# Kernel tuning notes

Hardware: AMD Instinct MI355X
Metric: run time of the kernel (lower is better)

Reference implementation:

```python
import jax, jax.numpy as jnp
import numpy as np


def setup_inputs() -> dict:
    key = jax.random.key(0)
    k1, k2 = jax.random.split(key)
    B, Te, Td, D = 16, 1024, 1024, 1024
    encoder_outputs = jax.random.normal(k1, (B, Te, D), dtype=jnp.float32)
    decoder_outputs = jax.random.normal(k2, (B, Td, D), dtype=jnp.float32)
    return {"encoder_outputs": encoder_outputs, "decoder_outputs": decoder_outputs}


def reference(encoder_outputs, decoder_outputs):
    # Luong score: [B, Te, Td] = enc @ dec^T
    luong_score = jnp.einsum("bed,btd->bet", encoder_outputs, decoder_outputs)
    # softmax over encoder-time axis (axis=1), matching K.softmax(..., axis=1)
    attn = jax.nn.softmax(luong_score, axis=1)
    # context vector: sum over encoder time of enc * attn -> [B, Td, D]
    # (original materializes [B, Te, Td, D]; this einsum is the same math)
    encoder_vector = jnp.einsum("bed,bet->btd", encoder_outputs, attn)
    return jnp.concatenate([decoder_outputs, encoder_vector], axis=-1)
```

## Files before the change

### kernel.cpp

```cpp
#include <hip/hip_runtime.h>
#include <hip/hip_bf16.h>
#include <stdint.h>

typedef __bf16 bf16x8 __attribute__((ext_vector_type(8)));
typedef float f32x4 __attribute__((ext_vector_type(4)));

#define B_DIM 16
#define TD 1024
#define TE 1024
#define DD 1024

typedef __attribute__((address_space(1))) void as1_void;
typedef __attribute__((address_space(3))) void as3_void;

#define GLL16(gp, lp) \
  __builtin_amdgcn_global_load_lds((as1_void*)(gp), (as3_void*)(lp), 16, 0, 0)

#define SB __builtin_amdgcn_sched_barrier(0)
#define BAR()                      \
  do {                             \
    SB;                            \
    __builtin_amdgcn_s_barrier();  \
    SB;                            \
  } while (0)
#define VMW4()                                       \
  do {                                               \
    asm volatile("s_waitcnt vmcnt(4)" ::: "memory"); \
    SB;                                              \
  } while (0)

__device__ __forceinline__ uint32_t rne_bf16(float x) {
  uint32_t u = __builtin_bit_cast(uint32_t, x);
  return (u + 0x7FFFu + ((u >> 16) & 1u)) >> 16;
}

__device__ __forceinline__ void split2(float x, uint32_t& hi, uint32_t& lo) {
  uint32_t h = rne_bf16(x);
  float hf = __builtin_bit_cast(float, h << 16);
  hi = h;
  lo = rne_bf16(x - hf);
}

__global__ __launch_bounds__(256)
void p0a_split_dec(const float4* __restrict__ dec4, uint32_t* __restrict__ dhi,
                   uint32_t* __restrict__ dlo, float4* __restrict__ out4) {
  size_t g = (size_t)blockIdx.x * 256 + threadIdx.x;
#pragma unroll
  for (int s = 0; s < 8; ++s, g += 524288) {
    float4 v = dec4[g];
    uint32_t h0, l0, h1, l1, h2, l2, h3, l3;
    split2(v.x, h0, l0);
    split2(v.y, h1, l1);
    split2(v.z, h2, l2);
    split2(v.w, h3, l3);
    *(uint2*)&dhi[g * 2] = make_uint2(h0 | (h1 << 16), h2 | (h3 << 16));
    *(uint2*)&dlo[g * 2] = make_uint2(l0 | (l1 << 16), l2 | (l3 << 16));
    size_t row = g >> 8, col = g & 255;
    out4[row * 512 + col] = v;
  }
}

__global__ __launch_bounds__(256)
void p0b_split_enc(const float* __restrict__ enc, uint32_t* __restrict__ ehi,
                   uint32_t* __restrict__ elo, uint16_t* __restrict__ eT) {
  __shared__ uint16_t TT[64][65];
  const int tid = threadIdx.x;
  const int b = blockIdx.z;
  const int d0 = (blockIdx.x & 15) * 64, e0 = (blockIdx.x >> 4) * 64;
  const float* src = enc + (size_t)b * TE * DD;
#pragma unroll
  for (int s = 0; s < 4; ++s) {
    int c = tid + 256 * s;
    int row = c >> 4, c4 = c & 15;
    float4 v = *(const float4*)(src + (size_t)(e0 + row) * DD + d0 + c4 * 4);
    uint32_t h0, l0, h1, l1, h2, l2, h3, l3;
    split2(v.x, h0, l0);
    split2(v.y, h1, l1);
    split2(v.z, h2, l2);
    split2(v.w, h3, l3);
    size_t o = (((size_t)b * TE + e0 + row) * DD + d0 + c4 * 4) >> 1;
    *(uint2*)&ehi[o] = make_uint2(h0 | (h1 << 16), h2 | (h3 << 16));
    *(uint2*)&elo[o] = make_uint2(l0 | (l1 << 16), l2 | (l3 << 16));
    TT[row][c4 * 4 + 0] = (uint16_t)h0;
    TT[row][c4 * 4 + 1] = (uint16_t)h1;
    TT[row][c4 * 4 + 2] = (uint16_t)h2;
    TT[row][c4 * 4 + 3] = (uint16_t)h3;
  }
  __syncthreads();
#pragma unroll
  for (int s = 0; s < 4; ++s) {
    int c = tid + 256 * s;
    int d = c >> 4, e4 = c & 15;
    uint32_t w0 = (uint32_t)TT[e4 * 4 + 0][d] | ((uint32_t)TT[e4 * 4 + 1][d] << 16);
    uint32_t w1 = (uint32_t)TT[e4 * 4 + 2][d] | ((uint32_t)TT[e4 * 4 + 3][d] << 16);
    *(uint2*)&eT[((size_t)b * DD + d0 + d) * TE + e0 + e4 * 4] = make_uint2(w0, w1);
  }
}

template <int NSEG>
__global__ __launch_bounds__(512, 2)
void k_gemm256(const uint16_t* __restrict__ a0, const uint16_t* __restrict__ a1,
               const uint16_t* __restrict__ a2, const uint16_t* __restrict__ b0,
               const uint16_t* __restrict__ b1, const uint16_t* __restrict__ b2,
               float* __restrict__ out) {
  extern __shared__ char lds[];
  const int tid = threadIdx.x;
  const int lane = tid & 63, wave = tid >> 6;
  const int wr = wave >> 2, wc = wave & 3;
  const int lr = lane & 15, q = lane >> 4;

  const int id = blockIdx.x;
  const int swz = (id & 7) * 32 + (id >> 3);
  const int b = swz >> 4, mblk = (swz >> 2) & 3, nblk = swz & 3;
  const size_t bOff = (size_t)b << 20;
  const int mrow0 = mblk * 256, nrow0 = nblk * 256;
  constexpr int T = NSEG * 16;

  const uint16_t* aS0 = a0 + bOff + (size_t)mrow0 * 1024;
  const uint16_t* aS1 = a1 + bOff + (size_t)mrow0 * 1024;
  const uint16_t* aS2 = a2 + bOff + (size_t)mrow0 * 1024;
  const uint16_t* bS0 = b0 + bOff + (size_t)nrow0 * 1024;
  const uint16_t* bS1 = b1 + bOff + (size_t)nrow0 * 1024;
  const uint16_t* bS2 = b2 + bOff + (size_t)nrow0 * 1024;

  const int r8 = tid >> 3, c8 = tid & 7;
  const int laneOff = r8 * 1024 + ((c8 ^ (r8 & 7)) << 3);
  char* dTid = lds + tid * 16;

#define STAGE_OP(P0_, P1_, P2_, HALF_, TAU_, REGION_)                         \
  do {                                                                        \
    int sg_ = (NSEG == 3) ? ((TAU_) >> 4) : 0;                                \
    int kl_ = (TAU_) & 15;                                                    \
    const uint16_t* s_ =                                                      \
        ((NSEG == 3) ? (sg_ == 0 ? (P0_) : (sg_ == 1 ? (P1_) : (P2_)))        \
                     : (P0_)) +                                               \
        (size_t)(HALF_)*131072 + (kl_ << 6) + laneOff;                        \
    char* d_ = dTid + (REGION_)*16384;                                        \
    GLL16(s_, d_);                                                            \
    GLL16(s_ + 65536, d_ + 8192);                                             \
  } while (0)

  const int xr = (lr & 7) << 4;
  const int colx = (q * 16) ^ xr;
  const char* aRd0 = lds + (wr << 14) + lr * 128 + colx;
  const char* aRd1 = lds + (wr << 14) + lr * 128 + (colx ^ 64);
  const char* bRdB = lds + ((2 + (wc >> 1)) << 14) + (wc & 1) * 8192 + lr * 128;
  const char* bRd0 = bRdB + colx;
  const char* bRd1 = bRdB + (colx ^ 64);

  f32x4 acc[8][4] = {};
  bf16x8 a[8], bA[2], bB[2];

#define LDA_ALL(SRC_)                                    \
  do {                                                   \
    _Pragma("unroll") for (int mi = 0; mi < 8; ++mi)     \
        a[mi] = *(const bf16x8*)((SRC_) + mi * 2048);    \
  } while (0)
#define LDB2(SRC_, NB_, DST_)                               \
  do {                                                      \
    DST_[0] = *(const bf16x8*)((SRC_) + (NB_)*2048);        \
    DST_[1] = *(const bf16x8*)((SRC_) + ((NB_) + 1) * 2048);\
  } while (0)

  auto MFMAQ = [&](bf16x8* bb, int npair) {
#pragma unroll
    for (int u = 0; u < 2; ++u)
#pragma unroll
      for (int mi = 0; mi < 8; ++mi)
        acc[mi][npair * 2 + u] = __builtin_amdgcn_mfma_f32_16x16x32_bf16(
            a[mi], bb[u], acc[mi][npair * 2 + u], 0, 0, 0);
  };

  STAGE_OP(aS0, aS1, aS2, 0, 0, 0);
  STAGE_OP(aS0, aS1, aS2, 1, 0, 1);
  STAGE_OP(bS0, bS1, bS2, 0, 0, 2);
  STAGE_OP(bS0, bS1, bS2, 1, 0, 3);
  STAGE_OP(aS0, aS1, aS2, 0, 1, 4);
  STAGE_OP(aS0, aS1, aS2, 1, 1, 5);
  VMW4();
  BAR();

  int dir = 65536;
#pragma unroll 1
  for (int t = 0; t < T; ++t) {
    const int cur = t & 1, nxt = cur ^ 1;
    const int t1 = (t + 1 < T) ? t + 1 : t + 1 - T;
    const int t2 = (t + 2 < T) ? t + 2 : t + 2 - T;
    LDA_ALL(aRd0);
    LDB2(bRd0, 0, bA);
    LDB2(bRd0, 2, bB);
    STAGE_OP(bS0, bS1, bS2, 0, t1, nxt * 4 + 2);
    BAR();
    __builtin_amdgcn_s_setprio(1);
    MFMAQ(bA, 0);
    __builtin_amdgcn_s_setprio(0);
    BAR();
    STAGE_OP(bS0, bS1, bS2, 1, t1, nxt * 4 + 3);
    BAR();
    __builtin_amdgcn_s_setprio(1);
    MFMAQ(bB, 1);
    __builtin_amdgcn_s_setprio(0);
    BAR();
    LDA_ALL(aRd1);
    LDB2(bRd1, 0, bA);
    LDB2(bRd1, 2, bB);
    BAR();
    __builtin_amdgcn_s_setprio(1);
    MFMAQ(bB, 1);
    __builtin_amdgcn_s_setprio(0);
    BAR();
    STAGE_OP(aS0, aS1, aS2, 0, t2, cur * 4 + 0);
    STAGE_OP(aS0, aS1, aS2, 1, t2, cur * 4 + 1);
    VMW4();
    BAR();
    __builtin_amdgcn_s_setprio(1);
    MFMAQ(bA, 0);
    __builtin_amdgcn_s_setprio(0);
    BAR();
    aRd0 += dir;
    aRd1 += dir;
    bRd0 += dir;
    bRd1 += dir;
    dir = -dir;
  }
#undef STAGE_OP
#undef LDA_ALL
#undef LDB2

  float* outp = out + (size_t)b * TD * 2048 + 1024;
  const int m0 = mrow0 + wr * 128 + q * 4;
  const int n0 = nrow0 + wc * 64 + lr;
#pragma unroll
  for (int mi = 0; mi < 8; ++mi)
#pragma unroll
    for (int ni = 0; ni < 4; ++ni)
#pragma unroll
      for (int i = 0; i < 4; ++i)
        outp[(size_t)(m0 + mi * 16 + i) * 2048 + (n0 + ni * 16)] = acc[mi][ni][i];
}

__global__ __launch_bounds__(256)
void k2_softmax_v3(const float* __restrict__ out, uint16_t* __restrict__ P) {
  const int lane = threadIdx.x & 63;
  const int row = blockIdx.x * 4 + (threadIdx.x >> 6);
  const float* Srow = out + (size_t)row * 2048 + 1024;
  float4 v[4];
#pragma unroll
  for (int s = 0; s < 4; ++s) v[s] = *(const float4*)(Srow + lane * 4 + s * 256);
  float m = -1e30f;
#pragma unroll
  for (int s = 0; s < 4; ++s)
    m = fmaxf(m, fmaxf(fmaxf(v[s].x, v[s].y), fmaxf(v[s].z, v[s].w)));
#pragma unroll
  for (int o = 32; o > 0; o >>= 1) m = fmaxf(m, __shfl_xor(m, o));
  float e[16];
  float sum = 0.f;
#pragma unroll
  for (int s = 0; s < 4; ++s) {
    e[4 * s + 0] = __expf(v[s].x - m);
    e[4 * s + 1] = __expf(v[s].y - m);
    e[4 * s + 2] = __expf(v[s].z - m);
    e[4 * s + 3] = __expf(v[s].w - m);
    sum += e[4 * s + 0] + e[4 * s + 1] + e[4 * s + 2] + e[4 * s + 3];
  }
#pragma unroll
  for (int o = 32; o > 0; o >>= 1) sum += __shfl_xor(sum, o);
  const float inv = 1.0f / sum;
  uint32_t* Prow = (uint32_t*)(P + (size_t)row * 1024);
#pragma unroll
  for (int s = 0; s < 4; ++s) {
    uint32_t r0 = rne_bf16(e[4 * s + 0] * inv);
    uint32_t r1 = rne_bf16(e[4 * s + 1] * inv);
    uint32_t r2 = rne_bf16(e[4 * s + 2] * inv);
    uint32_t r3 = rne_bf16(e[4 * s + 3] * inv);
    *(uint2*)&Prow[lane * 2 + s * 128] =
        make_uint2(r0 | (r1 << 16), r2 | (r3 << 16));
  }
}

__global__ __launch_bounds__(256, 2)
void k1_scores(const float* __restrict__ dec, const float* __restrict__ enc,
               float* __restrict__ out) {
  __shared__ uint32_t AhU[2048], AlU[2048], BhU[2048], BlU[2048];
  const int tid = threadIdx.x;
  const int lane = tid & 63;
  const int wave = tid >> 6;
  const int wm = wave >> 1, wn = wave & 1;
  const int b = blockIdx.z;
  const int t0 = blockIdx.y * 128, e0 = blockIdx.x * 128;
  const float* A = dec + (size_t)b * TD * DD;
  const float* Bm = enc + (size_t)b * TE * DD;

  const int r = tid >> 3, c4 = tid & 7;
  const float* aptr = A + (size_t)(t0 + r) * DD + c4 * 4;
  const float* bptr = Bm + (size_t)(e0 + r) * DD + c4 * 4;

  const int lr = lane & 15, q = lane >> 4;
  int aoff[4], boff[4];
#pragma unroll
  for (int i = 0; i < 4; ++i) {
    aoff[i] = (wm * 64 + i * 16 + lr) * 16 + q * 4;
    boff[i] = (wn * 64 + i * 16 + lr) * 16 + q * 4;
  }

  f32x4 acc[4][4] = {};

  for (int k0 = 0; k0 < DD; k0 += 32) {
#pragma unroll
    for (int s = 0; s < 4; ++s) {
      const float4 va = *(const float4*)(aptr + (size_t)(32 * s) * DD);
      const float4 vb = *(const float4*)(bptr + (size_t)(32 * s) * DD);
      const int woff = (r + 32 * s) * 16 + c4 * 2;
      {
        uint32_t u0 = __builtin_bit_cast(uint32_t, va.x);
        uint32_t u1 = __builtin_bit_cast(uint32_t, va.y);
        uint32_t u2 = __builtin_bit_cast(uint32_t, va.z);
        uint32_t u3 = __builtin_bit_cast(uint32_t, va.w);
        uint32_t m0 = u0 & 0xFFFF0000u, m1 = u1 & 0xFFFF0000u;
        uint32_t m2 = u2 & 0xFFFF0000u, m3 = u3 & 0xFFFF0000u;
        float l0 = va.x - __builtin_bit_cast(float, m0);
        float l1 = va.y - __builtin_bit_cast(float, m1);
        float l2 = va.z - __builtin_bit_cast(float, m2);
        float l3 = va.w - __builtin_bit_cast(float, m3);
        *(uint2*)&AhU[woff] = make_uint2((m0 >> 16) | m1, (m2 >> 16) | m3);
        *(uint2*)&AlU[woff] = make_uint2(
            (__builtin_bit_cast(uint32_t, l0) >> 16) |
                (__builtin_bit_cast(uint32_t, l1) & 0xFFFF0000u),
            (__builtin_bit_cast(uint32_t, l2) >> 16) |
                (__builtin_bit_cast(uint32_t, l3) & 0xFFFF0000u));
      }
      {
        uint32_t u0 = __builtin_bit_cast(uint32_t, vb.x);
        uint32_t u1 = __builtin_bit_cast(uint32_t, vb.y);
        uint32_t u2 = __builtin_bit_cast(uint32_t, vb.z);
        uint32_t u3 = __builtin_bit_cast(uint32_t, vb.w);
        uint32_t m0 = u0 & 0xFFFF0000u, m1 = u1 & 0xFFFF0000u;
        uint32_t m2 = u2 & 0xFFFF0000u, m3 = u3 & 0xFFFF0000u;
        float l0 = vb.x - __builtin_bit_cast(float, m0);
        float l1 = vb.y - __builtin_bit_cast(float, m1);
        float l2 = vb.z - __builtin_bit_cast(float, m2);
        float l3 = vb.w - __builtin_bit_cast(float, m3);
        *(uint2*)&BhU[woff] = make_uint2((m0 >> 16) | m1, (m2 >> 16) | m3);
        *(uint2*)&BlU[woff] = make_uint2(
            (__builtin_bit_cast(uint32_t, l0) >> 16) |
                (__builtin_bit_cast(uint32_t, l1) & 0xFFFF0000u),
            (__builtin_bit_cast(uint32_t, l2) >> 16) |
                (__builtin_bit_cast(uint32_t, l3) & 0xFFFF0000u));
      }
    }
    __syncthreads();

    bf16x8 ah[4], al[4];
#pragma unroll
    for (int mi = 0; mi < 4; ++mi) {
      ah[mi] = *(const bf16x8*)&AhU[aoff[mi]];
      al[mi] = *(const bf16x8*)&AlU[aoff[mi]];
    }
#pragma unroll
    for (int ni = 0; ni < 4; ++ni) {
      bf16x8 bh = *(const bf16x8*)&BhU[boff[ni]];
      bf16x8 bl = *(const bf16x8*)&BlU[boff[ni]];
#pragma unroll
      for (int mi = 0; mi < 4; ++mi) {
        f32x4 c = acc[mi][ni];
        c = __builtin_amdgcn_mfma_f32_16x16x32_bf16(al[mi], bh, c, 0, 0, 0);
        c = __builtin_amdgcn_mfma_f32_16x16x32_bf16(ah[mi], bl, c, 0, 0, 0);
        c = __builtin_amdgcn_mfma_f32_16x16x32_bf16(ah[mi], bh, c, 0, 0, 0);
        acc[mi][ni] = c;
      }
    }
    __syncthreads();
    aptr += 32;
    bptr += 32;
  }

  float* outb = out + (size_t)b * TD * 2048 + 1024;
  const int tb = t0 + wm * 64 + q * 4;
  const int eb = e0 + wn * 64 + lr;
#pragma unroll
  for (int mi = 0; mi < 4; ++mi)
#pragma unroll
    for (int ni = 0; ni < 4; ++ni)
#pragma unroll
      for (int i = 0; i < 4; ++i)
        outb[(size_t)(tb + mi * 16 + i) * 2048 + (eb + ni * 16)] = acc[mi][ni][i];
}

__global__ __launch_bounds__(256)
void k2_softmax(float* out) {
  const int lane = threadIdx.x & 63;
  const int row = blockIdx.x * 4 + (threadIdx.x >> 6);
  float* Srow = out + (size_t)row * 2048 + 1024;
  float4 v[4];
#pragma unroll
  for (int s = 0; s < 4; ++s) v[s] = *(const float4*)(Srow + lane * 4 + s * 256);
  float m = -1e30f;
#pragma unroll
  for (int s = 0; s < 4; ++s)
    m = fmaxf(m, fmaxf(fmaxf(v[s].x, v[s].y), fmaxf(v[s].z, v[s].w)));
#pragma unroll
  for (int o = 32; o > 0; o >>= 1) m = fmaxf(m, __shfl_xor(m, o));
  float e[16];
  float sum = 0.f;
#pragma unroll
  for (int s = 0; s < 4; ++s) {
    e[4 * s + 0] = __expf(v[s].x - m);
    e[4 * s + 1] = __expf(v[s].y - m);
    e[4 * s + 2] = __expf(v[s].z - m);
    e[4 * s + 3] = __expf(v[s].w - m);
    sum += e[4 * s + 0] + e[4 * s + 1] + e[4 * s + 2] + e[4 * s + 3];
  }
#pragma unroll
  for (int o = 32; o > 0; o >>= 1) sum += __shfl_xor(sum, o);
  const float inv = 1.0f / sum;
  uint32_t* Prow = (uint32_t*)(out + (size_t)row * 2048);
#pragma unroll
  for (int s = 0; s < 4; ++s) {
    uint32_t r0 = rne_bf16(e[4 * s + 0] * inv);
    uint32_t r1 = rne_bf16(e[4 * s + 1] * inv);
    uint32_t r2 = rne_bf16(e[4 * s + 2] * inv);
    uint32_t r3 = rne_bf16(e[4 * s + 3] * inv);
    *(uint2*)&Prow[lane * 2 + s * 128] =
        make_uint2(r0 | (r1 << 16), r2 | (r3 << 16));
  }
}

__global__ __launch_bounds__(256, 2)
void k3_av(const float* __restrict__ enc, float* __restrict__ out) {
  __shared__ uint32_t AU[2048];
  __shared__ uint32_t BtU[128 * 20];
  const int tid = threadIdx.x;
  const int lane = tid & 63, wave = tid >> 6;
  const int wm = wave >> 1, wn = wave & 1;
  const int b = blockIdx.z;
  const int t0 = blockIdx.y * 128, d0 = blockIdx.x * 128;
  const float* V = enc + (size_t)b * TE * DD;
  const uint16_t* Pb = (const uint16_t*)(out + (size_t)b * TD * 2048);
  const int lr = lane & 15, q = lane >> 4;
  int aoff[4], boff[4];
#pragma unroll
  for (int i = 0; i < 4; ++i) {
    aoff[i] = (wm * 64 + i * 16 + lr) * 16 + q * 4;
    boff[i] = (wn * 64 + i * 16 + lr) * 20 + q * 4;
  }
  const int dB = tid & 127;
  f32x4 acc[4][4] = {};

  for (int e0k = 0; e0k < TE; e0k += 32) {
#pragma unroll
    for (int s = 0; s < 2; ++s) {
      int c = tid + 256 * s;
      int rc = c >> 2, cc = c & 3;
      uint4 va = *(const uint4*)(Pb + (size_t)(t0 + rc) * 4096 + e0k + cc * 8);
      *(uint4*)&AU[c * 4] = va;
    }
#pragma unroll
    for (int s = 0; s < 4; ++s) {
      int eg = (tid >> 7) + 2 * s;
      const float* src = V + (size_t)(e0k + eg * 4) * DD + d0 + dB;
      float x0 = src[0], x1 = src[DD], x2 = src[2 * DD], x3 = src[3 * DD];
      uint32_t r0 = rne_bf16(x0), r1 = rne_bf16(x1);
      uint32_t r2 = rne_bf16(x2), r3 = rne_bf16(x3);
      *(uint2*)&BtU[dB * 20 + eg * 2] =
          make_uint2(r0 | (r1 << 16), r2 | (r3 << 16));
    }
    __syncthreads();

    bf16x8 af[4];
#pragma unroll
    for (int mi = 0; mi < 4; ++mi) af[mi] = *(const bf16x8*)&AU[aoff[mi]];
#pragma unroll
    for (int ni = 0; ni < 4; ++ni) {
      bf16x8 bfr = *(const bf16x8*)&BtU[boff[ni]];
#pragma unroll
      for (int mi = 0; mi < 4; ++mi)
        acc[mi][ni] =
            __builtin_amdgcn_mfma_f32_16x16x32_bf16(af[mi], bfr, acc[mi][ni], 0, 0, 0);
    }
    __syncthreads();
  }

  float* outb = out + (size_t)b * TD * 2048 + 1024;
  const int tb = t0 + wm * 64 + q * 4;
  const int db = d0 + wn * 64 + lr;
#pragma unroll
  for (int mi = 0; mi < 4; ++mi)
#pragma unroll
    for (int ni = 0; ni < 4; ++ni)
#pragma unroll
      for (int i = 0; i < 4; ++i)
        outb[(size_t)(tb + mi * 16 + i) * 2048 + (db + ni * 16)] = acc[mi][ni][i];
}

__global__ __launch_bounds__(256)
void k4_copydec(const float4* __restrict__ dec4, float4* __restrict__ out4) {
  size_t g = (size_t)blockIdx.x * 512 + threadIdx.x;
#pragma unroll
  for (int s = 0; s < 2; ++s, g += 256) {
    size_t row = g >> 8, col = g & 255;
    out4[row * 512 + col] = dec4[g];
  }
}

extern "C" void kernel_launch(void* const* d_in, const int* in_sizes, int n_in,
                              void* d_out, int out_size, void* d_ws, size_t ws_size,
                              hipStream_t stream) {
  const float* enc = (const float*)d_in[0];
  const float* dec = (const float*)d_in[1];
  float* out = (float*)d_out;

  const size_t M32 = 32ull << 20;
  bool fast = (d_ws != nullptr) && (ws_size >= 5 * M32);
  if (fast) {
    hipError_t e1 = hipFuncSetAttribute(
        (const void*)k_gemm256<3>, hipFuncAttributeMaxDynamicSharedMemorySize,
        131072);
    hipError_t e2 = hipFuncSetAttribute(
        (const void*)k_gemm256<1>, hipFuncAttributeMaxDynamicSharedMemorySize,
        131072);
    if (e1 != hipSuccess || e2 != hipSuccess) fast = false;
  }

  if (fast) {
    char* ws = (char*)d_ws;
    uint16_t* dhi = (uint16_t*)(ws);
    uint16_t* dlo = (uint16_t*)(ws + M32);
    uint16_t* ehi = (uint16_t*)(ws + 2 * M32);
    uint16_t* elo = (uint16_t*)(ws + 3 * M32);
    uint16_t* eT = (uint16_t*)(ws + 4 * M32);
    uint16_t* P = dhi;

    hipLaunchKernelGGL(p0a_split_dec, dim3(2048), dim3(256), 0, stream,
                       (const float4*)dec, (uint32_t*)dhi, (uint32_t*)dlo,
                       (float4*)out);
    hipLaunchKernelGGL(p0b_split_enc, dim3(256, 1, 16), dim3(256), 0, stream,
                       enc, (uint32_t*)ehi, (uint32_t*)elo, eT);
    hipLaunchKernelGGL(k_gemm256<3>, dim3(256), dim3(512), 131072, stream,
                       dhi, dhi, dlo, ehi, elo, ehi, out);
    hipLaunchKernelGGL(k2_softmax_v3, dim3(4096), dim3(256), 0, stream, out, P);
    hipLaunchKernelGGL(k_gemm256<1>, dim3(256), dim3(512), 131072, stream,
                       P, P, P, eT, eT, eT, out);
  } else {
    hipLaunchKernelGGL(k1_scores, dim3(8, 8, 16), dim3(256), 0, stream, dec, enc, out);
    hipLaunchKernelGGL(k2_softmax, dim3(4096), dim3(256), 0, stream, out);
    hipLaunchKernelGGL(k3_av, dim3(8, 8, 16), dim3(256), 0, stream, enc, out);
    hipLaunchKernelGGL(k4_copydec, dim3(8192), dim3(256), 0, stream,
                       (const float4*)dec, (float4*)out);
  }
}
```

Baseline: 400.6 us.

## Double-buffer LDS-to-register fragments to overlap reads with MFMA

Splits the A and B register fragments into two sets so the next k-half's LDS reads are issued before the current MFMA quadrant runs. The next iteration's first fragments are loaded right after the global-to-LDS wait. This is meant to hide LDS read latency behind matrix-core work instead of stalling at the start of each phase. The cost is roughly 40 extra VGPRs per thread under a 512-thread, 2-blocks-per-CU launch bound, which risks spills or lower occupancy.

```diff
diff --git a/kernel.cpp b/kernel.cpp
--- a/kernel.cpp
+++ b/kernel.cpp
@@ -99,9 +99,9 @@
 
 template <int NSEG>
 __global__ __launch_bounds__(512, 2)
-void k_gemm256(const uint16_t* __restrict__ a0, const uint16_t* __restrict__ a1,
-               const uint16_t* __restrict__ a2, const uint16_t* __restrict__ b0,
-               const uint16_t* __restrict__ b1, const uint16_t* __restrict__ b2,
+void k_gemm256(const uint16_t* __restrict__ a0p, const uint16_t* __restrict__ a1p,
+               const uint16_t* __restrict__ a2p, const uint16_t* __restrict__ b0p,
+               const uint16_t* __restrict__ b1p, const uint16_t* __restrict__ b2p,
                float* __restrict__ out) {
   extern __shared__ char lds[];
   const int tid = threadIdx.x;
@@ -116,12 +116,12 @@
   const int mrow0 = mblk * 256, nrow0 = nblk * 256;
   constexpr int T = NSEG * 16;
 
-  const uint16_t* aS0 = a0 + bOff + (size_t)mrow0 * 1024;
-  const uint16_t* aS1 = a1 + bOff + (size_t)mrow0 * 1024;
-  const uint16_t* aS2 = a2 + bOff + (size_t)mrow0 * 1024;
-  const uint16_t* bS0 = b0 + bOff + (size_t)nrow0 * 1024;
-  const uint16_t* bS1 = b1 + bOff + (size_t)nrow0 * 1024;
-  const uint16_t* bS2 = b2 + bOff + (size_t)nrow0 * 1024;
+  const uint16_t* aS0 = a0p + bOff + (size_t)mrow0 * 1024;
+  const uint16_t* aS1 = a1p + bOff + (size_t)mrow0 * 1024;
+  const uint16_t* aS2 = a2p + bOff + (size_t)mrow0 * 1024;
+  const uint16_t* bS0 = b0p + bOff + (size_t)nrow0 * 1024;
+  const uint16_t* bS1 = b1p + bOff + (size_t)nrow0 * 1024;
+  const uint16_t* bS2 = b2p + bOff + (size_t)nrow0 * 1024;
 
   const int r8 = tid >> 3, c8 = tid & 7;
   const int laneOff = r8 * 1024 + ((c8 ^ (r8 & 7)) << 3);
@@ -149,12 +149,12 @@
   const char* bRd1 = bRdB + (colx ^ 64);
 
   f32x4 acc[8][4] = {};
-  bf16x8 a[8], bA[2], bB[2];
-
-#define LDA_ALL(SRC_)                                    \
+  bf16x8 a0[8], a1[8], bA0[2], bB0[2], bA1[2], bB1[2];
+
+#define LDA_ALL(SRC_, DST_)                              \
   do {                                                   \
     _Pragma("unroll") for (int mi = 0; mi < 8; ++mi)     \
-        a[mi] = *(const bf16x8*)((SRC_) + mi * 2048);    \
+        DST_[mi] = *(const bf16x8*)((SRC_) + mi * 2048); \
   } while (0)
 #define LDB2(SRC_, NB_, DST_)                               \
   do {                                                      \
@@ -162,13 +162,13 @@
     DST_[1] = *(const bf16x8*)((SRC_) + ((NB_) + 1) * 2048);\
   } while (0)
 
-  auto MFMAQ = [&](bf16x8* bb, int npair) {
+  auto MFMAQ = [&](const bf16x8* aa, const bf16x8* bb, int npair) {
 #pragma unroll
     for (int u = 0; u < 2; ++u)
 #pragma unroll
       for (int mi = 0; mi < 8; ++mi)
         acc[mi][npair * 2 + u] = __builtin_amdgcn_mfma_f32_16x16x32_bf16(
-            a[mi], bb[u], acc[mi][npair * 2 + u], 0, 0, 0);
+            aa[mi], bb[u], acc[mi][npair * 2 + u], 0, 0, 0);
   };
 
   STAGE_OP(aS0, aS1, aS2, 0, 0, 0);
@@ -179,6 +179,8 @@
   STAGE_OP(aS0, aS1, aS2, 1, 1, 5);
   VMW4();
   BAR();
+  LDA_ALL(aRd0, a0);
+  LDB2(bRd0, 0, bA0);
 
   int dir = 65536;
 #pragma unroll 1
@@ -186,35 +188,35 @@
     const int cur = t & 1, nxt = cur ^ 1;
     const int t1 = (t + 1 < T) ? t + 1 : t + 1 - T;
     const int t2 = (t + 2 < T) ? t + 2 : t + 2 - T;
-    LDA_ALL(aRd0);
-    LDB2(bRd0, 0, bA);
-    LDB2(bRd0, 2, bB);
+    LDB2(bRd0, 2, bB0);
     STAGE_OP(bS0, bS1, bS2, 0, t1, nxt * 4 + 2);
     BAR();
     __builtin_amdgcn_s_setprio(1);
-    MFMAQ(bA, 0);
+    MFMAQ(a0, bA0, 0);
     __builtin_amdgcn_s_setprio(0);
     BAR();
+    LDA_ALL(aRd1, a1);
+    LDB2(bRd1, 2, bB1);
     STAGE_OP(bS0, bS1, bS2, 1, t1, nxt * 4 + 3);
     BAR();
     __builtin_amdgcn_s_setprio(1);
-    MFMAQ(bB, 1);
+    MFMAQ(a0, bB0, 1);
     __builtin_amdgcn_s_setprio(0);
     BAR();
-    LDA_ALL(aRd1);
-    LDB2(bRd1, 0, bA);
-    LDB2(bRd1, 2, bB);
+    LDB2(bRd1, 0, bA1);
     BAR();
     __builtin_amdgcn_s_setprio(1);
-    MFMAQ(bB, 1);
+    MFMAQ(a1, bB1, 1);
     __builtin_amdgcn_s_setprio(0);
     BAR();
     STAGE_OP(aS0, aS1, aS2, 0, t2, cur * 4 + 0);
     STAGE_OP(aS0, aS1, aS2, 1, t2, cur * 4 + 1);
     VMW4();
     BAR();
+    LDA_ALL(aRd0 + dir, a0);
+    LDB2(bRd0 + dir, 0, bA0);
     __builtin_amdgcn_s_setprio(1);
-    MFMAQ(bA, 0);
+    MFMAQ(a1, bA1, 0);
     __builtin_amdgcn_s_setprio(0);
     BAR();
     aRd0 += dir;
```

New measurement: 394.1 us. Within noise of the previous version (-1.6%).
